# Performance work log

Hardware: AMD Instinct MI355X
Metric: run time of the kernel (lower is better)

## Reference

```python
import jax, jax.numpy as jnp
import numpy as np
import math

B, S, E, H = 2, 2048, 1024, 16
D = E // H  # d_head = 64

def setup_inputs() -> dict:
    key = jax.random.key(0)
    ks = jax.random.split(key, 7)
    query = jax.random.normal(ks[0], (B, S, E), dtype=jnp.float32)
    k_in = jax.random.normal(ks[1], (B, S, E), dtype=jnp.float32)
    v_in = jax.random.normal(ks[2], (B, S, E), dtype=jnp.float32)
    # causal mask, broadcastable over batch and heads; mask==0 positions are blocked
    mask = jnp.tril(jnp.ones((S, S), dtype=jnp.int32))[None, None]
    scale = 1.0 / math.sqrt(E)
    w_q = jax.random.normal(ks[3], (E, E), dtype=jnp.float32) * scale
    w_k = jax.random.normal(ks[4], (E, E), dtype=jnp.float32) * scale
    w_v = jax.random.normal(ks[5], (E, E), dtype=jnp.float32) * scale
    w_o = jax.random.normal(ks[6], (E, E), dtype=jnp.float32) * scale
    return {"query": query, "key": k_in, "value": v_in, "mask": mask,
            "w_q": w_q, "w_k": w_k, "w_v": w_v, "w_o": w_o}

def reference(query, key, value, mask, w_q, w_k, w_v, w_o):
    # projections (nn.Linear with no bias: x @ W^T); split heads -> [B,H,S,D]
    q = (query @ w_q.T).reshape(B, S, H, D).transpose(0, 2, 1, 3)
    k = (key @ w_k.T).reshape(B, S, H, D).transpose(0, 2, 1, 3)
    v = (value @ w_v.T).reshape(B, S, H, D).transpose(0, 2, 1, 3)
    # scaled dot-product scores [B,H,S,S]
    scores = jnp.einsum('bhqd,bhkd->bhqk', q, k) / math.sqrt(D)
    scores = jnp.where(mask == 0, jnp.float32(-1e9), scores)
    attn = jax.nn.softmax(scores, axis=-1)  # dropout p=0.0 -> identity
    out = jnp.einsum('bhqk,bhkd->bhqd', attn, v)  # [B,H,S,D]
    out = out.transpose(0, 2, 1, 3).reshape(B, S, E)
    return out @ w_o.T
```

## Files before the change

### kernel.cpp

```cpp
#include <hip/hip_runtime.h>
#include <hip/hip_bf16.h>

#define B_ 2
#define S_ 2048
#define E_ 1024
#define H_ 16
#define D_ 64

typedef __attribute__((ext_vector_type(8))) short bf16x8;
typedef __attribute__((ext_vector_type(4))) float f32x4;

static __device__ __forceinline__ unsigned short f2bf(float x) {
    union { float f; unsigned u; } v; v.f = x;
    unsigned r = v.u + 0x7FFF + ((v.u >> 16) & 1);
    return (unsigned short)(r >> 16);
}

static __device__ __forceinline__ unsigned pack2bf(float a, float b) {
    union { float f; unsigned u; } x, y; x.f = a; y.f = b;
    unsigned ra = x.u + 0x7FFF + ((x.u >> 16) & 1);
    unsigned rb = y.u + 0x7FFF + ((y.u >> 16) & 1);
    return (ra >> 16) | (rb & 0xFFFF0000u);
}

static __device__ __forceinline__ unsigned packtrunc(float a, float b) {
    union { float f; unsigned u; } x, y; x.f = a; y.f = b;
    return __builtin_amdgcn_perm(y.u, x.u, 0x07060302);
}

static __device__ __forceinline__ void async_copy16(const void* gsrc, void* ldst) {
    __builtin_amdgcn_global_load_lds(
        (const __attribute__((address_space(1))) void*)gsrc,
        (__attribute__((address_space(3))) void*)ldst, 16, 0, 0);
}

__global__ void cvt_all(const float* __restrict__ s0, const float* __restrict__ s1,
                        const float* __restrict__ s2, const float* __restrict__ s3,
                        const float* __restrict__ s4, const float* __restrict__ s5,
                        const float* __restrict__ s6,
                        unsigned short* __restrict__ xdst, unsigned short* __restrict__ wdst,
                        float scq) {
    int b = blockIdx.x;
    const float* src; unsigned short* dst; int i; float c = 1.f;
    if (b < 12288) {
        int ti = b >> 12, lb = b & 4095;
        src = (ti == 0) ? s0 : (ti == 1) ? s1 : s2;
        dst = xdst + (size_t)ti * 4194304;
        i = lb * 256 + threadIdx.x;
    } else {
        int r = b - 12288, ti = r >> 10, lb = r & 1023;
        src = (ti == 0) ? s3 : (ti == 1) ? s4 : (ti == 2) ? s5 : s6;
        dst = wdst + (size_t)ti * 1048576;
        i = lb * 256 + threadIdx.x;
        if (ti == 0) c = scq;
    }
    float4 f = ((const float4*)src)[i];
    ushort4 o;
    o.x = f2bf(f.x * c); o.y = f2bf(f.y * c); o.z = f2bf(f.z * c); o.w = f2bf(f.w * c);
    ((ushort4*)dst)[i] = o;
}

__global__ __launch_bounds__(512, 2) void gemm256(
    const unsigned short* __restrict__ A0, const unsigned short* __restrict__ B0,
    void* __restrict__ C0) {
    __shared__ __align__(16) unsigned short L[65536];
    const int z = blockIdx.z;
    const unsigned short* A  = A0 + (size_t)z * 4194304;
    const unsigned short* Bm = B0 + (size_t)z * 1048576;
    const int o = (int)(blockIdx.x + (blockIdx.y << 2));
    const int cx = o & 7, tx = o >> 3;
    const int bm = (cx * 2 + (tx >> 2)) * 256;
    const int bn = (tx & 3) * 256;
    const int tid = threadIdx.x;
    const int w = tid >> 6, lane = tid & 63;
    const int wr = w >> 2, wc = w & 3;
    const int col = lane & 15, quad = lane >> 4;
    const int r0 = tid >> 3, cg = (tid & 7) ^ (r0 & 7);
    const size_t aR = (size_t)(bm + r0) * 1024 + cg * 8;
    const size_t bR = (size_t)(bn + r0) * 1024 + cg * 8;
    const int l0 = tid * 8, l1 = tid * 8 + 4096;
    const int ach = (quad ^ (col & 7)) * 8;
    const int aRd = wr * 8192 + col * 64 + ach;
    const int bRd = 32768 + (wc >> 1) * 8192 + (wc & 1) * 4096 + col * 64 + ach;

    f32x4 acc[8][4] = {};
    bf16x8 bA[4][2], bB0[2][2], bB1[2][2];

#define STAGE_A(d, h, t) do { \
    async_copy16(A + aR + (size_t)((h) * 128) * 1024 + (t) * 64, &L[((d) * 2 + (h)) * 8192 + l0]); \
    async_copy16(A + aR + (size_t)((h) * 128 + 64) * 1024 + (t) * 64, &L[((d) * 2 + (h)) * 8192 + l1]); \
} while (0)
#define STAGE_B(d, h, t) do { \
    async_copy16(Bm + bR + (size_t)((h) * 128) * 1024 + (t) * 64, &L[32768 + ((d) * 2 + (h)) * 8192 + l0]); \
    async_copy16(Bm + bR + (size_t)((h) * 128 + 64) * 1024 + (t) * 64, &L[32768 + ((d) * 2 + (h)) * 8192 + l1]); \
} while (0)
#define RD_A(d, mh) do { _Pragma("unroll") for (int i = 0; i < 4; i++) { \
    bA[i][0] = *(const bf16x8*)&L[(d) * 16384 + (mh) * 4096 + i * 1024 + aRd]; \
    bA[i][1] = *(const bf16x8*)&L[(d) * 16384 + (mh) * 4096 + i * 1024 + (aRd ^ 32)]; } } while (0)
#define RD_B(d, nh, BB) do { _Pragma("unroll") for (int j = 0; j < 2; j++) { \
    BB[j][0] = *(const bf16x8*)&L[(d) * 16384 + (nh) * 2048 + j * 1024 + bRd]; \
    BB[j][1] = *(const bf16x8*)&L[(d) * 16384 + (nh) * 2048 + j * 1024 + (bRd ^ 32)]; } } while (0)
#define MM(m0, BB, n0) do { __builtin_amdgcn_s_setprio(1); \
    _Pragma("unroll") for (int i = 0; i < 4; i++) _Pragma("unroll") for (int j = 0; j < 2; j++) { \
        acc[(m0) + i][(n0) + j] = __builtin_amdgcn_mfma_f32_16x16x32_bf16(bA[i][0], BB[j][0], acc[(m0) + i][(n0) + j], 0, 0, 0); \
        acc[(m0) + i][(n0) + j] = __builtin_amdgcn_mfma_f32_16x16x32_bf16(bA[i][1], BB[j][1], acc[(m0) + i][(n0) + j], 0, 0, 0); } \
    __builtin_amdgcn_s_setprio(0); } while (0)
#define BARX __builtin_amdgcn_s_barrier()
#define VMW asm volatile("s_waitcnt vmcnt(4)" ::: "memory")

    STAGE_B(0, 0, 0); STAGE_B(0, 1, 0);
    STAGE_A(0, 0, 0); STAGE_A(0, 1, 0);
    STAGE_B(1, 0, 1); STAGE_B(1, 1, 1);
    VMW; BARX;

#pragma unroll 1
    for (int j = 0; j < 8; j++) {
        const int to = 2 * j + 1;
        const int tn = (2 * j + 2 < 16) ? 2 * j + 2 : 15;
        const int tm = (2 * j + 3 < 16) ? 2 * j + 3 : 15;
        STAGE_A(1, 0, to); RD_A(0, 0); RD_B(0, 0, bB0); BARX; MM(0, bB0, 0); BARX;
        STAGE_A(1, 1, to); RD_B(0, 1, bB1);             BARX; MM(0, bB1, 2); BARX;
        STAGE_B(0, 0, tn); RD_A(0, 1);                  BARX; MM(4, bB1, 2); BARX;
        STAGE_B(0, 1, tn);                              BARX; MM(4, bB0, 0); VMW; BARX;
        STAGE_A(0, 0, tn); RD_A(1, 0); RD_B(1, 0, bB0); BARX; MM(0, bB0, 0); BARX;
        STAGE_A(0, 1, tn); RD_B(1, 1, bB1);             BARX; MM(0, bB1, 2); BARX;
        STAGE_B(1, 0, tm); RD_A(1, 1);                  BARX; MM(4, bB1, 2); BARX;
        STAGE_B(1, 1, tm);                              BARX; MM(4, bB0, 0); VMW; BARX;
    }
#undef STAGE_A
#undef STAGE_B
#undef RD_A
#undef RD_B
#undef MM
#undef BARX
#undef VMW

    __syncthreads();

    unsigned short* scr = &L[w * 8192];
    const int grow0 = bm + wr * 128;
    const int b  = grow0 >> 11;
    const int s0 = grow0 & 2047;
    const int hh = (bn + wc * 64) >> 6;
    unsigned short* outp = (unsigned short*)C0 + (size_t)z * 4194304;
    if (z == 2) {
#pragma unroll
        for (int mi = 0; mi < 8; mi++)
#pragma unroll
            for (int nj = 0; nj < 4; nj++) {
                int n = nj * 16 + col;
                int c = mi * 2 + (quad >> 1);
                uint2 pk;
                pk.x = pack2bf(acc[mi][nj][0], acc[mi][nj][1]);
                pk.y = pack2bf(acc[mi][nj][2], acc[mi][nj][3]);
                *(uint2*)&scr[n * 128 + ((c ^ (n & 7)) << 3) + ((quad & 1) << 2)] = pk;
            }
        asm volatile("s_waitcnt lgkmcnt(0)" ::: "memory");
#pragma unroll
        for (int it = 0; it < 32; it++) {
            int slot = it * 64 + lane;
            int n = slot >> 5, u = slot & 31;
            int grp = u >> 3, T = u & 7;
            int kpos = grp * 32 + (T & 1) * 16 + ((T >> 1) & 3) * 4;
            int c = kpos >> 3, off = kpos & 7;
            uint2 v = *(uint2*)&scr[n * 128 + ((c ^ (n & 7)) << 3) + off];
            *(uint2*)&outp[(((size_t)b * H_ + hh) * D_ + n) * S_ + s0 + grp * 32 + T * 4] = v;
        }
    } else {
#pragma unroll
        for (int mi = 0; mi < 8; mi++)
#pragma unroll
            for (int nj = 0; nj < 4; nj++)
#pragma unroll
                for (int r = 0; r < 4; r++) {
                    int m = mi * 16 + quad * 4 + r, n = nj * 16 + col;
                    scr[m * 64 + (((n >> 3) ^ (m & 7)) << 3) + (n & 7)] = f2bf(acc[mi][nj][r]);
                }
        asm volatile("s_waitcnt lgkmcnt(0)" ::: "memory");
#pragma unroll
        for (int it = 0; it < 16; it++) {
            int slot = it * 64 + lane, m = slot >> 3, c = slot & 7;
            uint4 v = *(uint4*)&scr[m * 64 + ((c ^ (m & 7)) << 3)];
            *(uint4*)&outp[(((size_t)b * H_ + hh) * S_ + s0 + m) * (size_t)D_ + c * 8] = v;
        }
    }
}

__global__ __launch_bounds__(512) void gemmO(
    const unsigned short* __restrict__ A0, const unsigned short* __restrict__ B0,
    float* __restrict__ C0) {
    __shared__ __align__(16) unsigned short KV[8][4096];
    const int o = (int)(blockIdx.x + (blockIdx.y << 3));
    const int cx = o & 7, tx = o >> 3;
    const int bm = ((cx << 2) + (tx >> 3)) * 128;
    const int bn = (tx & 7) * 128;
    const int tid = threadIdx.x;
    const int w = tid >> 6, lane = tid & 63;
    const int col = lane & 15, quad = lane >> 4;
    const int wm = (w >> 1) * 32, wn = (w & 1) * 64;
    const int cq = (quad ^ ((col >> 1) & 3)) << 3;

    f32x4 acc[2][4] = {};

    const int r0 = tid >> 2;
    const int cg = (tid & 3) ^ ((r0 >> 1) & 3);
    const size_t aoff = (size_t)(bm + r0) * 1024 + cg * 8;
    const size_t boff = (size_t)(bn + r0) * 1024 + cg * 8;
    const int l0 = tid * 8;

    const int nk = 32;
    async_copy16(A0 + aoff,      &KV[0][l0]);
    async_copy16(B0 + boff,      &KV[4][l0]);
    async_copy16(A0 + aoff + 32, &KV[1][l0]);
    async_copy16(B0 + boff + 32, &KV[5][l0]);

#pragma unroll 1
    for (int kt = 0; kt < nk; kt++) {
        const int kp = kt + 2;
        const int src = (kp < nk) ? kp : (nk - 1);
        const int bp = kp & 3;
        async_copy16(A0 + aoff + (size_t)src * 32, &KV[bp][l0]);
        async_copy16(B0 + boff + (size_t)src * 32, &KV[4 + bp][l0]);
        asm volatile("s_waitcnt vmcnt(4)" ::: "memory");
        __builtin_amdgcn_s_barrier();

        const unsigned short* Ab = &KV[kt & 3][0];
        const unsigned short* Bb = &KV[4 + (kt & 3)][0];
        bf16x8 af[2], bfr[4];
#pragma unroll
        for (int i = 0; i < 2; i++) af[i]  = *(const bf16x8*)&Ab[(wm + i * 16 + col) * 32 + cq];
#pragma unroll
        for (int j = 0; j < 4; j++) bfr[j] = *(const bf16x8*)&Bb[(wn + j * 16 + col) * 32 + cq];
#pragma unroll
        for (int i = 0; i < 2; i++)
#pragma unroll
            for (int j = 0; j < 4; j++)
                acc[i][j] = __builtin_amdgcn_mfma_f32_16x16x32_bf16(af[i], bfr[j], acc[i][j], 0, 0, 0);
    }

    __syncthreads();

#pragma unroll
    for (int i = 0; i < 2; i++)
#pragma unroll
        for (int j = 0; j < 4; j++)
#pragma unroll
            for (int r = 0; r < 4; r++) {
                int gm = bm + wm + i * 16 + quad * 4 + r;
                int gn = bn + wn + j * 16 + col;
                C0[(size_t)gm * 1024 + gn] = acc[i][j][r];
            }
}

__global__ __launch_bounds__(512, 4) void attn_kernel(
    const unsigned short* __restrict__ Q, const unsigned short* __restrict__ K_,
    const unsigned short* __restrict__ Vt, unsigned short* __restrict__ Out) {
    __shared__ __align__(16) unsigned short KV[8][4096];
    __shared__ __align__(16) float Lred[4][2][64];
    const int o = (int)(blockIdx.x + (blockIdx.y << 4));
    const int cx = o & 7, tx = o >> 3;
    const int hloc = (tx >> 1) & 3;
    const int f_ = (tx ^ (tx >> 5)) & 1;
    const int G_ = (((tx >> 4) & 1) << 2) | (((tx >> 3) & 1) << 1) | (tx & 1);
    const int qb = f_ ? (G_ ^ 15) : G_;
    const int bh = (cx << 2) + hloc;
    const int q0 = qb * 128;
    const int tid = threadIdx.x;
    const int w = tid >> 6, lane = tid & 63;
    const int qg = w >> 1, kh = w & 1, kh32 = kh << 5;
    const int col = lane & 15, quad = lane >> 4, swz = col & 7;
    const int qw0 = q0 + qg * 32;
    const float NINF = -__builtin_huge_valf();

    const unsigned short* Qh = Q + (size_t)bh * S_ * D_;
    const unsigned short* Kh = K_ + (size_t)bh * S_ * D_;
    const unsigned short* Vh = Vt + (size_t)bh * D_ * S_;

    bf16x8 qf[2][2];
#pragma unroll
    for (int i = 0; i < 2; i++)
#pragma unroll
        for (int h = 0; h < 2; h++)
            qf[i][h] = *(const bf16x8*)(Qh + (size_t)(qw0 + i * 16 + col) * 64 + h * 32 + quad * 8);

    f32x4 o_[2][4] = {};
    float lsum[2] = {0.f, 0.f};
    f32x4 scA[2][2], scB[2][2];

    const int sRow = tid >> 3, sCg = (tid & 7) ^ (sRow & 7);
    const size_t koff = (size_t)sRow * 64 + sCg * 8;
    const size_t voff = (size_t)sRow * S_ + sCg * 8;
    const int ldsoff = tid * 8;
    const int vch = ((kh * 4 + quad) ^ (col & 7)) << 3;

    const int nk = 2 * (qb + 1);

    async_copy16(Kh + koff, &KV[0][ldsoff]);
    async_copy16(Kh + koff + 4096, &KV[1][ldsoff]);
    async_copy16(Vh + voff, &KV[4][ldsoff]);

#define APROC(T, PRV) do { \
    const int k0p = (T) * 64; \
    if (k0p + kh32 + 31 <= qw0) { \
        _Pragma("unroll") for (int i2 = 0; i2 < 2; i2++) \
        _Pragma("unroll") for (int c2 = 0; c2 < 2; c2++) { \
            _Pragma("unroll") for (int r2 = 0; r2 < 4; r2++) \
                PRV[i2][c2][r2] = __builtin_amdgcn_exp2f(PRV[i2][c2][r2]); \
            lsum[i2] += (PRV[i2][c2][0] + PRV[i2][c2][1]) + (PRV[i2][c2][2] + PRV[i2][c2][3]); } \
    } else { \
        _Pragma("unroll") for (int i2 = 0; i2 < 2; i2++) \
        _Pragma("unroll") for (int c2 = 0; c2 < 2; c2++) { \
            _Pragma("unroll") for (int r2 = 0; r2 < 4; r2++) { \
                int key = k0p + kh32 + c2 * 16 + quad * 4 + r2; \
                int qidx = qw0 + i2 * 16 + col; \
                float sv = (key <= qidx) ? PRV[i2][c2][r2] : NINF; \
                PRV[i2][c2][r2] = __builtin_amdgcn_exp2f(sv); } \
            lsum[i2] += (PRV[i2][c2][0] + PRV[i2][c2][1]) + (PRV[i2][c2][2] + PRV[i2][c2][3]); } \
    } \
    union { bf16x8 v; unsigned u[4]; } pf[2]; \
    _Pragma("unroll") for (int i2 = 0; i2 < 2; i2++) { \
        pf[i2].u[0] = packtrunc(PRV[i2][0][0], PRV[i2][0][1]); \
        pf[i2].u[1] = packtrunc(PRV[i2][0][2], PRV[i2][0][3]); \
        pf[i2].u[2] = packtrunc(PRV[i2][1][0], PRV[i2][1][1]); \
        pf[i2].u[3] = packtrunc(PRV[i2][1][2], PRV[i2][1][3]); } \
    const unsigned short* Vbp = &KV[4 + ((T) & 3)][0]; \
    __builtin_amdgcn_s_setprio(1); \
    _Pragma("unroll") for (int dt = 0; dt < 4; dt++) { \
        bf16x8 vf = *(const bf16x8*)&Vbp[(dt * 16 + col) * 64 + vch]; \
        _Pragma("unroll") for (int i2 = 0; i2 < 2; i2++) \
            o_[i2][dt] = __builtin_amdgcn_mfma_f32_16x16x32_bf16(vf, pf[i2].v, o_[i2][dt], 0, 0, 0); } \
    __builtin_amdgcn_s_setprio(0); \
} while (0)

#define AITER(KT, CUR, PRV, DOPRV) do { \
    const int kti = (KT); \
    { const int kp = kti + 2; const int srcK = (kp < nk) ? kp : (nk - 1); \
      async_copy16(Kh + koff + (size_t)srcK * 4096, &KV[kp & 3][ldsoff]); \
      const int vp = kti + 1; const int srcV = (vp < nk) ? vp : (nk - 1); \
      async_copy16(Vh + voff + (size_t)srcV * 64, &KV[4 + (vp & 3)][ldsoff]); } \
    asm volatile("s_waitcnt vmcnt(4)" ::: "memory"); \
    __builtin_amdgcn_s_barrier(); \
    if (kti * 64 + kh32 <= qw0 + 31) { \
        const unsigned short* Kb = &KV[kti & 3][0]; \
        _Pragma("unroll") for (int i2 = 0; i2 < 2; i2++) \
        _Pragma("unroll") for (int c2 = 0; c2 < 2; c2++) \
        _Pragma("unroll") for (int r2 = 0; r2 < 4; r2++) CUR[i2][c2][r2] = 0.f; \
        __builtin_amdgcn_s_setprio(1); \
        _Pragma("unroll") for (int h = 0; h < 2; h++) { \
            const int cqh = ((h * 4 + quad) ^ swz) * 8; \
            _Pragma("unroll") for (int ct = 0; ct < 2; ct++) { \
                bf16x8 kf = *(const bf16x8*)&Kb[(kh32 + ct * 16 + col) * 64 + cqh]; \
                CUR[0][ct] = __builtin_amdgcn_mfma_f32_16x16x32_bf16(kf, qf[0][h], CUR[0][ct], 0, 0, 0); \
                CUR[1][ct] = __builtin_amdgcn_mfma_f32_16x16x32_bf16(kf, qf[1][h], CUR[1][ct], 0, 0, 0); } } \
        __builtin_amdgcn_s_setprio(0); \
    } \
    if ((DOPRV) && (kti - 1) * 64 + kh32 <= qw0 + 31) APROC(kti - 1, PRV); \
} while (0)

    AITER(0, scA, scB, 0);
    AITER(1, scB, scA, 1);
#pragma unroll 1
    for (int kt = 2; kt < nk; kt += 2) {
        AITER(kt, scA, scB, 1);
        AITER(kt + 1, scB, scA, 1);
    }
    asm volatile("s_waitcnt vmcnt(0)" ::: "memory");
    __builtin_amdgcn_s_barrier();
    if ((nk - 1) * 64 + kh32 <= qw0 + 31) APROC(nk - 1, scB);
#undef AITER
#undef APROC

    __syncthreads();
    if (kh == 1) {
        f32x4* R = (f32x4*)&KV[0][0] + qg * 512 + lane * 8;
#pragma unroll
        for (int i = 0; i < 2; i++)
#pragma unroll
            for (int dt = 0; dt < 4; dt++) R[i * 4 + dt] = o_[i][dt];
        Lred[qg][0][lane] = lsum[0];
        Lred[qg][1][lane] = lsum[1];
    }
    __syncthreads();
    if (kh == 0) {
        f32x4* R = (f32x4*)&KV[0][0] + qg * 512 + lane * 8;
#pragma unroll
        for (int i = 0; i < 2; i++)
#pragma unroll
            for (int dt = 0; dt < 4; dt++) o_[i][dt] += R[i * 4 + dt];
        lsum[0] += Lred[qg][0][lane];
        lsum[1] += Lred[qg][1][lane];

        const int b = bh >> 4, hh = bh & 15;
#pragma unroll
        for (int i = 0; i < 2; i++) {
            float l = lsum[i];
            l += __shfl_xor(l, 16);
            l += __shfl_xor(l, 32);
            float inv = 1.f / l;
            int gq = qw0 + i * 16 + col;
#pragma unroll
            for (int dt = 0; dt < 4; dt++) {
                uint2 pk;
                pk.x = pack2bf(o_[i][dt][0] * inv, o_[i][dt][1] * inv);
                pk.y = pack2bf(o_[i][dt][2] * inv, o_[i][dt][3] * inv);
                *(uint2*)&Out[((size_t)b * S_ + gq) * E_ + hh * 64 + dt * 16 + quad * 4] = pk;
            }
        }
    }
}

extern "C" void kernel_launch(void* const* d_in, const int* in_sizes, int n_in,
                              void* d_out, int out_size, void* d_ws, size_t ws_size,
                              hipStream_t stream) {
    const float* query = (const float*)d_in[0];
    const float* key_i = (const float*)d_in[1];
    const float* value = (const float*)d_in[2];
    const float* w_q = (const float*)d_in[4];
    const float* w_k = (const float*)d_in[5];
    const float* w_v = (const float*)d_in[6];
    const float* w_o = (const float*)d_in[7];
    float* out = (float*)d_out;

    char* ws = (char*)d_ws;
    unsigned short* xq  = (unsigned short*)(ws);
    unsigned short* wqb = (unsigned short*)(ws + (24u << 20));
    unsigned short* Qb  = (unsigned short*)(ws + (32u << 20));
    unsigned short* Kb  = (unsigned short*)(ws + (40u << 20));
    unsigned short* Vtb = (unsigned short*)(ws + (48u << 20));
    unsigned short* Ab  = (unsigned short*)(ws + (56u << 20));

    const float SCQ = 0.125f * 1.44269504088896f;

    cvt_all<<<16384, 256, 0, stream>>>(query, key_i, value, w_q, w_k, w_v, w_o,
                                       xq, wqb, SCQ);

    gemm256<<<dim3(4, 16, 3), 512, 0, stream>>>(xq, wqb, Qb);

    attn_kernel<<<dim3(S_ / 128, B_ * H_), 512, 0, stream>>>(Qb, Kb, Vtb, Ab);

    gemmO<<<dim3(8, 32), 512, 0, stream>>>(Ab, wqb + 3u * 1048576u, out);
}
```

Measured before the change: 196.6 us.

## Replace 256x256 QKV GEMM with 128x128-tile 4-stage pipelined kernel

```diff
diff --git a/kernel.cpp b/kernel.cpp
--- a/kernel.cpp
+++ b/kernel.cpp
@@ -60,128 +60,96 @@
     ((ushort4*)dst)[i] = o;
 }
 
-__global__ __launch_bounds__(512, 2) void gemm256(
+__global__ __launch_bounds__(512) void gemmQKV(
     const unsigned short* __restrict__ A0, const unsigned short* __restrict__ B0,
-    void* __restrict__ C0) {
-    __shared__ __align__(16) unsigned short L[65536];
+    unsigned short* __restrict__ C0) {
+    __shared__ __align__(16) unsigned short KV[8][4096];
     const int z = blockIdx.z;
     const unsigned short* A  = A0 + (size_t)z * 4194304;
     const unsigned short* Bm = B0 + (size_t)z * 1048576;
-    const int o = (int)(blockIdx.x + (blockIdx.y << 2));
+    const int o = (int)(blockIdx.x + (blockIdx.y << 3));
     const int cx = o & 7, tx = o >> 3;
-    const int bm = (cx * 2 + (tx >> 2)) * 256;
-    const int bn = (tx & 3) * 256;
+    const int bm = ((cx << 2) + (tx >> 3)) * 128;
+    const int bn = (tx & 7) * 128;
     const int tid = threadIdx.x;
     const int w = tid >> 6, lane = tid & 63;
-    const int wr = w >> 2, wc = w & 3;
     const int col = lane & 15, quad = lane >> 4;
-    const int r0 = tid >> 3, cg = (tid & 7) ^ (r0 & 7);
-    const size_t aR = (size_t)(bm + r0) * 1024 + cg * 8;
-    const size_t bR = (size_t)(bn + r0) * 1024 + cg * 8;
-    const int l0 = tid * 8, l1 = tid * 8 + 4096;
-    const int ach = (quad ^ (col & 7)) * 8;
-    const int aRd = wr * 8192 + col * 64 + ach;
-    const int bRd = 32768 + (wc >> 1) * 8192 + (wc & 1) * 4096 + col * 64 + ach;
-
-    f32x4 acc[8][4] = {};
-    bf16x8 bA[4][2], bB0[2][2], bB1[2][2];
-
-#define STAGE_A(d, h, t) do { \
-    async_copy16(A + aR + (size_t)((h) * 128) * 1024 + (t) * 64, &L[((d) * 2 + (h)) * 8192 + l0]); \
-    async_copy16(A + aR + (size_t)((h) * 128 + 64) * 1024 + (t) * 64, &L[((d) * 2 + (h)) * 8192 + l1]); \
-} while (0)
-#define STAGE_B(d, h, t) do { \
-    async_copy16(Bm + bR + (size_t)((h) * 128) * 1024 + (t) * 64, &L[32768 + ((d) * 2 + (h)) * 8192 + l0]); \
-    async_copy16(Bm + bR + (size_t)((h) * 128 + 64) * 1024 + (t) * 64, &L[32768 + ((d) * 2 + (h)) * 8192 + l1]); \
-} while (0)
-#define RD_A(d, mh) do { _Pragma("unroll") for (int i = 0; i < 4; i++) { \
-    bA[i][0] = *(const bf16x8*)&L[(d) * 16384 + (mh) * 4096 + i * 1024 + aRd]; \
-    bA[i][1] = *(const bf16x8*)&L[(d) * 16384 + (mh) * 4096 + i * 1024 + (aRd ^ 32)]; } } while (0)
-#define RD_B(d, nh, BB) do { _Pragma("unroll") for (int j = 0; j < 2; j++) { \
-    BB[j][0] = *(const bf16x8*)&L[(d) * 16384 + (nh) * 2048 + j * 1024 + bRd]; \
-    BB[j][1] = *(const bf16x8*)&L[(d) * 16384 + (nh) * 2048 + j * 1024 + (bRd ^ 32)]; } } while (0)
-#define MM(m0, BB, n0) do { __builtin_amdgcn_s_setprio(1); \
-    _Pragma("unroll") for (int i = 0; i < 4; i++) _Pragma("unroll") for (int j = 0; j < 2; j++) { \
-        acc[(m0) + i][(n0) + j] = __builtin_amdgcn_mfma_f32_16x16x32_bf16(bA[i][0], BB[j][0], acc[(m0) + i][(n0) + j], 0, 0, 0); \
-        acc[(m0) + i][(n0) + j] = __builtin_amdgcn_mfma_f32_16x16x32_bf16(bA[i][1], BB[j][1], acc[(m0) + i][(n0) + j], 0, 0, 0); } \
-    __builtin_amdgcn_s_setprio(0); } while (0)
-#define BARX __builtin_amdgcn_s_barrier()
-#define VMW asm volatile("s_waitcnt vmcnt(4)" ::: "memory")
-
-    STAGE_B(0, 0, 0); STAGE_B(0, 1, 0);
-    STAGE_A(0, 0, 0); STAGE_A(0, 1, 0);
-    STAGE_B(1, 0, 1); STAGE_B(1, 1, 1);
-    VMW; BARX;
+    const int wm = (w >> 1) * 32, wn = (w & 1) * 64;
+    const int cq = (quad ^ ((col >> 1) & 3)) << 3;
+
+    f32x4 acc[2][4] = {};
+
+    const int r0 = tid >> 2;
+    const int cg = (tid & 3) ^ ((r0 >> 1) & 3);
+    const size_t aoff = (size_t)(bm + r0) * 1024 + cg * 8;
+    const size_t boff = (size_t)(bn + r0) * 1024 + cg * 8;
+    const int l0 = tid * 8;
+
+    const int nk = 32;
+    async_copy16(A  + aoff,      &KV[0][l0]);
+    async_copy16(Bm + boff,      &KV[4][l0]);
+    async_copy16(A  + aoff + 32, &KV[1][l0]);
+    async_copy16(Bm + boff + 32, &KV[5][l0]);
 
 #pragma unroll 1
-    for (int j = 0; j < 8; j++) {
-        const int to = 2 * j + 1;
-        const int tn = (2 * j + 2 < 16) ? 2 * j + 2 : 15;
-        const int tm = (2 * j + 3 < 16) ? 2 * j + 3 : 15;
-        STAGE_A(1, 0, to); RD_A(0, 0); RD_B(0, 0, bB0); BARX; MM(0, bB0, 0); BARX;
-        STAGE_A(1, 1, to); RD_B(0, 1, bB1);             BARX; MM(0, bB1, 2); BARX;
-        STAGE_B(0, 0, tn); RD_A(0, 1);                  BARX; MM(4, bB1, 2); BARX;
-        STAGE_B(0, 1, tn);                              BARX; MM(4, bB0, 0); VMW; BARX;
-        STAGE_A(0, 0, tn); RD_A(1, 0); RD_B(1, 0, bB0); BARX; MM(0, bB0, 0); BARX;
-        STAGE_A(0, 1, tn); RD_B(1, 1, bB1);             BARX; MM(0, bB1, 2); BARX;
-        STAGE_B(1, 0, tm); RD_A(1, 1);                  BARX; MM(4, bB1, 2); BARX;
-        STAGE_B(1, 1, tm);                              BARX; MM(4, bB0, 0); VMW; BARX;
-    }
-#undef STAGE_A
-#undef STAGE_B
-#undef RD_A
-#undef RD_B
-#undef MM
-#undef BARX
-#undef VMW
+    for (int kt = 0; kt < nk; kt++) {
+        const int kp = kt + 2;
+        const int src = (kp < nk) ? kp : (nk - 1);
+        const int bp = kp & 3;
+        async_copy16(A  + aoff + (size_t)src * 32, &KV[bp][l0]);
+        async_copy16(Bm + boff + (size_t)src * 32, &KV[4 + bp][l0]);
+        asm volatile("s_waitcnt vmcnt(4)" ::: "memory");
+        __builtin_amdgcn_s_barrier();
+
+        const unsigned short* Ab = &KV[kt & 3][0];
+        const unsigned short* Bb = &KV[4 + (kt & 3)][0];
+        bf16x8 af[2], bfr[4];
+#pragma unroll
+        for (int i = 0; i < 2; i++) af[i]  = *(const bf16x8*)&Ab[(wm + i * 16 + col) * 32 + cq];
+#pragma unroll
+        for (int j = 0; j < 4; j++) bfr[j] = *(const bf16x8*)&Bb[(wn + j * 16 + col) * 32 + cq];
+#pragma unroll
+        for (int i = 0; i < 2; i++)
+#pragma unroll
+            for (int j = 0; j < 4; j++)
+                acc[i][j] = __builtin_amdgcn_mfma_f32_16x16x32_bf16(af[i], bfr[j], acc[i][j], 0, 0, 0);
+    }
 
     __syncthreads();
 
-    unsigned short* scr = &L[w * 8192];
-    const int grow0 = bm + wr * 128;
-    const int b  = grow0 >> 11;
-    const int s0 = grow0 & 2047;
-    const int hh = (bn + wc * 64) >> 6;
-    unsigned short* outp = (unsigned short*)C0 + (size_t)z * 4194304;
+    unsigned short* outp = C0 + (size_t)z * 4194304;
+    const int gm0 = bm + wm;
+    const int b  = gm0 >> 11;
+    const int s0g = gm0 & 2047;
+    const int hh = (bn + wn) >> 6;
     if (z == 2) {
 #pragma unroll
-        for (int mi = 0; mi < 8; mi++)
-#pragma unroll
-            for (int nj = 0; nj < 4; nj++) {
-                int n = nj * 16 + col;
-                int c = mi * 2 + (quad >> 1);
+        for (int i = 0; i < 2; i++)
+#pragma unroll
+            for (int j = 0; j < 4; j++) {
+                int d = j * 16 + col;
                 uint2 pk;
-                pk.x = pack2bf(acc[mi][nj][0], acc[mi][nj][1]);
-                pk.y = pack2bf(acc[mi][nj][2], acc[mi][nj][3]);
-                *(uint2*)&scr[n * 128 + ((c ^ (n & 7)) << 3) + ((quad & 1) << 2)] = pk;
+                pk.x = pack2bf(acc[i][j][0], acc[i][j][1]);
+                pk.y = pack2bf(acc[i][j][2], acc[i][j][3]);
+                *(uint2*)&outp[(((size_t)b * H_ + hh) * D_ + d) * S_ + s0g + (i + quad * 2) * 4] = pk;
             }
-        asm volatile("s_waitcnt lgkmcnt(0)" ::: "memory");
-#pragma unroll
-        for (int it = 0; it < 32; it++) {
-            int slot = it * 64 + lane;
-            int n = slot >> 5, u = slot & 31;
-            int grp = u >> 3, T = u & 7;
-            int kpos = grp * 32 + (T & 1) * 16 + ((T >> 1) & 3) * 4;
-            int c = kpos >> 3, off = kpos & 7;
-            uint2 v = *(uint2*)&scr[n * 128 + ((c ^ (n & 7)) << 3) + off];
-            *(uint2*)&outp[(((size_t)b * H_ + hh) * D_ + n) * S_ + s0 + grp * 32 + T * 4] = v;
-        }
     } else {
-#pragma unroll
-        for (int mi = 0; mi < 8; mi++)
-#pragma unroll
-            for (int nj = 0; nj < 4; nj++)
+        unsigned short* scr = &KV[w][0];
+#pragma unroll
+        for (int i = 0; i < 2; i++)
+#pragma unroll
+            for (int j = 0; j < 4; j++)
 #pragma unroll
                 for (int r = 0; r < 4; r++) {
-                    int m = mi * 16 + quad * 4 + r, n = nj * 16 + col;
-                    scr[m * 64 + (((n >> 3) ^ (m & 7)) << 3) + (n & 7)] = f2bf(acc[mi][nj][r]);
+                    int m = i * 16 + quad * 4 + r, n = j * 16 + col;
+                    scr[m * 64 + (((n >> 3) ^ (m & 7)) << 3) + (n & 7)] = f2bf(acc[i][j][r]);
                 }
         asm volatile("s_waitcnt lgkmcnt(0)" ::: "memory");
 #pragma unroll
-        for (int it = 0; it < 16; it++) {
+        for (int it = 0; it < 4; it++) {
             int slot = it * 64 + lane, m = slot >> 3, c = slot & 7;
             uint4 v = *(uint4*)&scr[m * 64 + ((c ^ (m & 7)) << 3)];
-            *(uint4*)&outp[(((size_t)b * H_ + hh) * S_ + s0 + m) * (size_t)D_ + c * 8] = v;
+            *(uint4*)&outp[(((size_t)b * H_ + hh) * S_ + s0g + m) * (size_t)D_ + c * 8] = v;
         }
     }
 }
@@ -434,7 +402,7 @@
     cvt_all<<<16384, 256, 0, stream>>>(query, key_i, value, w_q, w_k, w_v, w_o,
                                        xq, wqb, SCQ);
 
-    gemm256<<<dim3(4, 16, 3), 512, 0, stream>>>(xq, wqb, Qb);
+    gemmQKV<<<dim3(8, 32, 3), 512, 0, stream>>>(xq, wqb, Qb);
 
     attn_kernel<<<dim3(S_ / 128, B_ * H_), 512, 0, stream>>>(Qb, Kb, Vtb, Ab);
 
```

Measured after the change: 199.6 us. About the same (+1.5%).
